# Optimization experiments

Hardware: AMD Instinct MI355X
Metric: run time of the kernel (lower is better)

The kernel has to match this reference:

```python
import jax, jax.numpy as jnp
import numpy as np

N, A, R = 131072, 16, 64


def setup_inputs() -> dict:
    key = jax.random.key(0)
    k1, k2, k3 = jax.random.split(key, 3)
    x = jax.random.normal(k1, (N, A), dtype=jnp.float32)
    mu = jax.random.uniform(k2, (R, A), dtype=jnp.float32)      # torch.rand(R, A)
    sigma = jnp.ones((R, A), dtype=jnp.float32) * 0.2           # torch.ones(R, A) * 0.2
    rho = jax.random.normal(k3, (R, A + 1), dtype=jnp.float32) * 0.1
    return {"x": x, "mu": mu, "sigma": sigma, "rho": rho}


def reference(x, mu, sigma, rho):
    # Rule consequents: z[k, r] = x[k] . rho[r, :A] + rho[r, A]   -> [N, R]
    z = jnp.einsum("na,ra->nr", x, rho[:, :-1]) + rho[:, -1]
    # Gaussian membership firing strengths (prod of exps == exp of sum):
    # w[k, r] = prod_a exp(-(x[k,a]-mu[r,a])^2 / (2 sigma[r,a]^2))
    d = x[:, None, :] - mu[None, :, :]                           # [N, R, A]
    logw = -jnp.sum(d * d / (2.0 * sigma[None] ** 2), axis=-1)   # [N, R]
    w = jnp.exp(logw)
    # diag(z @ w.T)[k] = sum_r z[k,r] * w[k,r]; normalized by rule-sum.
    num = jnp.sum(z * w, axis=1)
    den = jnp.sum(w, axis=1) + 1e-13
    return num / den
```

## Files before the change

### kernel.cpp

```cpp
#include <hip/hip_runtime.h>
#include <math.h>

#define NFEAT 16
#define NRULE 64
#define NCHUNK 19
#define FLAG_DW (NCHUNK * 64 * 4)

typedef _Float16 half8 __attribute__((ext_vector_type(8)));
typedef float    f4    __attribute__((ext_vector_type(4)));
union F4H8 { float4 f; half8 h; };
union F4A  { float4 v; float f[4]; };

__global__ void fuzzy_prep(const float* __restrict__ mu,
                           const float* __restrict__ sigma,
                           const float* __restrict__ rho,
                           float* __restrict__ tab) {
    const float L2E = 1.4426950408889634f;
    __shared__ int u_sh[256];
    int t = threadIdx.x;
    int L = t & 63, T = t >> 6;
    int n = L & 15, quad = L >> 4;
    int rule = T * 16 + n;
    int fb = (quad & 1) * 8;

    F4A M[4], S[4];
    const float4* mup = (const float4*)(mu + rule * NFEAT);
    const float4* sgp = (const float4*)(sigma + rule * NFEAT);
#pragma unroll
    for (int i = 0; i < 4; ++i) { M[i].v = mup[i]; S[i].v = sgp[i]; }

    F4H8 b1, b2, r1, r2;
#pragma unroll
    for (int j = 0; j < 8; ++j) {
        int f = fb + j;
        float m = M[f >> 2].f[f & 3];
        float s = S[f >> 2].f[f & 3];
        float inv = 1.0f / (2.0f * s * s);
        float Bw = 2.0f * inv * m * L2E;
        _Float16 bh = (_Float16)Bw;
        b1.h[j] = bh;
        b2.h[j] = (_Float16)(Bw - (float)bh);
        float Rw = rho[rule * (NFEAT + 1) + f];
        _Float16 rh = (_Float16)Rw;
        r1.h[j] = rh;
        r2.h[j] = (_Float16)(Rw - (float)rh);
    }
    float4* t4 = (float4*)tab;
    t4[(0  + T) * 64 + L] = b1.f;
    t4[(4  + T) * 64 + L] = b2.f;
    t4[(8  + T) * 64 + L] = r1.f;
    t4[(12 + T) * 64 + L] = r2.f;

    float s0 = S[0].f[0];
    float c0 = 1.0f / (2.0f * s0 * s0);
    float K = 0.0f;
    int u = 1;
#pragma unroll
    for (int a = 0; a < NFEAT; ++a) {
        float m = M[a >> 2].f[a & 3];
        float s = S[a >> 2].f[a & 3];
        float inv = 1.0f / (2.0f * s * s);
        if (inv != c0) u = 0;
        K = fmaf(-inv * m, m, K);
    }
    tab[(16 * 64 + L) * 4 + T] = -c0 * L2E;
    tab[(17 * 64 + L) * 4 + T] = K * L2E;
    tab[(18 * 64 + L) * 4 + T] = rho[rule * (NFEAT + 1) + NFEAT];

    u_sh[t] = u;
    __syncthreads();
    if (t < 64) {
        int uu = u_sh[t] & u_sh[t + 64] & u_sh[t + 128] & u_sh[t + 192];
        unsigned long long b = __ballot(uu != 0);
        if (t == 0) tab[FLAG_DW] = (b == ~0ull) ? 1.0f : 0.0f;
    }
}

__global__ __launch_bounds__(256, 4) void fuzzy_main(const float* __restrict__ x,
                                                     const float* __restrict__ tab,
                                                     const float* __restrict__ mu,
                                                     const float* __restrict__ sigma,
                                                     const float* __restrict__ rho,
                                                     float* __restrict__ out, int n) {
    const int tid  = threadIdx.x;
    const int L    = tid & 63;
    const int quad = L >> 4;
    const int wv   = __builtin_amdgcn_readfirstlane(tid >> 6);
    const int flag = __builtin_amdgcn_readfirstlane((int)tab[FLAG_DW]);
    const int m    = L & 15;
    const int fb   = (quad & 1) * 8;

    if (flag) {
        const float4* t4 = (const float4*)tab;
        F4H8 b1[4], b2[4], r1[4], r2[4];
#pragma unroll
        for (int T = 0; T < 4; ++T) {
            b1[T].f = t4[(0  + T) * 64 + L];
            b2[T].f = t4[(4  + T) * 64 + L];
            r1[T].f = t4[(8  + T) * 64 + L];
            r2[T].f = t4[(12 + T) * 64 + L];
        }
        float4 Pq = t4[16 * 64 + L], Kq = t4[17 * 64 + L], Bq = t4[18 * 64 + L];
        float PvA[4]  = {Pq.x, Pq.y, Pq.z, Pq.w};
        float KLvA[4] = {Kq.x, Kq.y, Kq.z, Kq.w};
        float BvA[4]  = {Bq.x, Bq.y, Bq.z, Bq.w};

#pragma unroll
        for (int it = 0; it < 2; ++it) {
            int gt = (blockIdx.x * 4 + wv) * 2 + it;
            int tb = gt * 16;
            if (tb >= n) break;
            const float4* xp = (const float4*)(x + (size_t)(tb + m) * NFEAT + fb);
            float4 xa = xp[0], xb = xp[1];
            float xv[8] = {xa.x, xa.y, xa.z, xa.w, xb.x, xb.y, xb.z, xb.w};
            F4H8 af;
            float qp = 0.0f;
#pragma unroll
            for (int j = 0; j < 8; ++j) {
                _Float16 h = (_Float16)xv[j];
                af.h[j] = (quad < 2) ? h : (_Float16)(xv[j] - (float)h);
                qp = fmaf(xv[j], xv[j], qp);
            }
            float Qf = qp + __shfl_xor(qp, 16);
            float Qr[4];
#pragma unroll
            for (int p = 0; p < 4; ++p) Qr[p] = __shfl(Qf, quad * 4 + p);

            f4 nsum = {0.f, 0.f, 0.f, 0.f}, dsum = {0.f, 0.f, 0.f, 0.f};
#pragma unroll
            for (int T = 0; T < 4; ++T) {
                f4 z4 = {0.f, 0.f, 0.f, 0.f};
                f4 accL = __builtin_amdgcn_mfma_f32_16x16x32_f16(af.h, b1[T].h, z4, 0, 0, 0);
                accL    = __builtin_amdgcn_mfma_f32_16x16x32_f16(af.h, b2[T].h, accL, 0, 0, 0);
                f4 accZ = __builtin_amdgcn_mfma_f32_16x16x32_f16(af.h, r1[T].h, z4, 0, 0, 0);
                accZ    = __builtin_amdgcn_mfma_f32_16x16x32_f16(af.h, r2[T].h, accZ, 0, 0, 0);
#pragma unroll
                for (int p = 0; p < 4; ++p) {
                    float l = fmaf(PvA[T], Qr[p], accL[p] + KLvA[T]);
                    float w = __builtin_amdgcn_exp2f(l);
                    float zf = accZ[p] + BvA[T];
                    nsum[p] = fmaf(zf, w, nsum[p]);
                    dsum[p] += w;
                }
            }
#pragma unroll
            for (int d = 1; d < 16; d <<= 1) {
#pragma unroll
                for (int p = 0; p < 4; ++p) {
                    nsum[p] += __shfl_xor(nsum[p], d);
                    dsum[p] += __shfl_xor(dsum[p], d);
                }
            }
            if ((L & 15) == 0) {
                float4 o;
                o.x = nsum[0] * __builtin_amdgcn_rcpf(dsum[0] + 1e-13f);
                o.y = nsum[1] * __builtin_amdgcn_rcpf(dsum[1] + 1e-13f);
                o.z = nsum[2] * __builtin_amdgcn_rcpf(dsum[2] + 1e-13f);
                o.w = nsum[3] * __builtin_amdgcn_rcpf(dsum[3] + 1e-13f);
                ((float4*)(out + tb))[quad] = o;
            }
        }
    } else {
        const float L2E = 1.4426950408889634f;
#pragma unroll
        for (int it = 0; it < 2; ++it) {
            int gt = (blockIdx.x * 4 + wv) * 2 + it;
            int tb = gt * 16;
            if (tb >= n) break;
            int s = tb + m;
            const float4* xp = (const float4*)(x + (size_t)s * NFEAT);
            float4 a = xp[0], b = xp[1], c = xp[2], d = xp[3];
            float xs[NFEAT] = {a.x,a.y,a.z,a.w, b.x,b.y,b.z,b.w,
                               c.x,c.y,c.z,c.w, d.x,d.y,d.z,d.w};
            float num = 0.0f, den = 0.0f;
            for (int r = quad * 16; r < quad * 16 + 16; ++r) {
                float z = rho[r * (NFEAT + 1) + NFEAT];
                float l = 0.0f;
                for (int aa = 0; aa < NFEAT; ++aa) {
                    float mm = mu[r * NFEAT + aa];
                    float ss = sigma[r * NFEAT + aa];
                    float inv = 1.0f / (2.0f * ss * ss);
                    float dd = xs[aa] - mm;
                    l = fmaf(-inv * dd, dd, l);
                    z = fmaf(rho[r * (NFEAT + 1) + aa], xs[aa], z);
                }
                float w = __builtin_amdgcn_exp2f(l * L2E);
                num = fmaf(z, w, num);
                den += w;
            }
            num += __shfl_xor(num, 16); den += __shfl_xor(den, 16);
            num += __shfl_xor(num, 32); den += __shfl_xor(den, 32);
            if (L < 16) out[tb + L] = num / (den + 1e-13f);
        }
    }
}

extern "C" void kernel_launch(void* const* d_in, const int* in_sizes, int n_in,
                              void* d_out, int out_size, void* d_ws, size_t ws_size,
                              hipStream_t stream) {
    const float* x     = (const float*)d_in[0];
    const float* mu    = (const float*)d_in[1];
    const float* sigma = (const float*)d_in[2];
    const float* rho   = (const float*)d_in[3];
    float* out = (float*)d_out;
    float* tab = (float*)d_ws;

    int n = in_sizes[0] / NFEAT;

    fuzzy_prep<<<1, 256, 0, stream>>>(mu, sigma, rho, tab);
    int blocks = (n + 127) / 128;
    fuzzy_main<<<blocks, 256, 0, stream>>>(x, tab, mu, sigma, rho, out, n);
}
```

Baseline: 70.51 us.

## Fuse parameter prep into main kernel via shared-memory tables

Removes the separate single-block prep kernel and its global workspace table. Each block now recomputes the split-fp16 coefficient tables and the uniform-sigma flag into shared memory, then runs the MFMA path. Samples per wave go from 2 to 4 tiles, which halves the block count and amortises the per-block prep. This saves one launch and the serialisation between the two kernels, at the cost of redundant prep work in every block and an extra barrier.

Result: slower. 74.21 us (+5.2%).

```diff
diff --git a/kernel.cpp b/kernel.cpp
--- a/kernel.cpp
+++ b/kernel.cpp
@@ -4,110 +4,106 @@
 #define NFEAT 16
 #define NRULE 64
 #define NCHUNK 19
-#define FLAG_DW (NCHUNK * 64 * 4)
+#define IT 4
 
 typedef _Float16 half8 __attribute__((ext_vector_type(8)));
 typedef float    f4    __attribute__((ext_vector_type(4)));
 union F4H8 { float4 f; half8 h; };
 union F4A  { float4 v; float f[4]; };
 
-__global__ void fuzzy_prep(const float* __restrict__ mu,
-                           const float* __restrict__ sigma,
-                           const float* __restrict__ rho,
-                           float* __restrict__ tab) {
+__global__ __launch_bounds__(256, 2) void fuzzy_all(const float* __restrict__ x,
+                                                    const float* __restrict__ mu,
+                                                    const float* __restrict__ sigma,
+                                                    const float* __restrict__ rho,
+                                                    float* __restrict__ out, int n) {
     const float L2E = 1.4426950408889634f;
+    __shared__ float4 sh4[NCHUNK * 64];
     __shared__ int u_sh[256];
-    int t = threadIdx.x;
-    int L = t & 63, T = t >> 6;
-    int n = L & 15, quad = L >> 4;
-    int rule = T * 16 + n;
-    int fb = (quad & 1) * 8;
-
-    F4A M[4], S[4];
-    const float4* mup = (const float4*)(mu + rule * NFEAT);
-    const float4* sgp = (const float4*)(sigma + rule * NFEAT);
-#pragma unroll
-    for (int i = 0; i < 4; ++i) { M[i].v = mup[i]; S[i].v = sgp[i]; }
-
-    F4H8 b1, b2, r1, r2;
-#pragma unroll
-    for (int j = 0; j < 8; ++j) {
-        int f = fb + j;
-        float m = M[f >> 2].f[f & 3];
-        float s = S[f >> 2].f[f & 3];
-        float inv = 1.0f / (2.0f * s * s);
-        float Bw = 2.0f * inv * m * L2E;
-        _Float16 bh = (_Float16)Bw;
-        b1.h[j] = bh;
-        b2.h[j] = (_Float16)(Bw - (float)bh);
-        float Rw = rho[rule * (NFEAT + 1) + f];
-        _Float16 rh = (_Float16)Rw;
-        r1.h[j] = rh;
-        r2.h[j] = (_Float16)(Rw - (float)rh);
+    __shared__ float flag_sh;
+
+    const int t    = threadIdx.x;
+    const int L    = t & 63;
+    const int T    = t >> 6;
+    const int m    = L & 15;
+    const int quad = L >> 4;
+    const int rule = T * 16 + m;
+    const int fb   = (quad & 1) * 8;
+
+    {
+        F4A M[4], S[4];
+        const float4* mup = (const float4*)(mu + rule * NFEAT);
+        const float4* sgp = (const float4*)(sigma + rule * NFEAT);
+#pragma unroll
+        for (int i = 0; i < 4; ++i) { M[i].v = mup[i]; S[i].v = sgp[i]; }
+
+        F4H8 b1, b2, r1, r2;
+#pragma unroll
+        for (int j = 0; j < 8; ++j) {
+            int f = fb + j;
+            float mm = M[f >> 2].f[f & 3];
+            float ss = S[f >> 2].f[f & 3];
+            float inv = 1.0f / (2.0f * ss * ss);
+            float Bw = 2.0f * inv * mm * L2E;
+            _Float16 bh = (_Float16)Bw;
+            b1.h[j] = bh;
+            b2.h[j] = (_Float16)(Bw - (float)bh);
+            float Rw = rho[rule * (NFEAT + 1) + f];
+            _Float16 rh = (_Float16)Rw;
+            r1.h[j] = rh;
+            r2.h[j] = (_Float16)(Rw - (float)rh);
+        }
+        sh4[(0  + T) * 64 + L] = b1.f;
+        sh4[(4  + T) * 64 + L] = b2.f;
+        sh4[(8  + T) * 64 + L] = r1.f;
+        sh4[(12 + T) * 64 + L] = r2.f;
+
+        float s0 = S[0].f[0];
+        float c0 = 1.0f / (2.0f * s0 * s0);
+        float K = 0.0f;
+        int u = 1;
+#pragma unroll
+        for (int a = 0; a < NFEAT; ++a) {
+            float mm = M[a >> 2].f[a & 3];
+            float ss = S[a >> 2].f[a & 3];
+            float inv = 1.0f / (2.0f * ss * ss);
+            if (inv != c0) u = 0;
+            K = fmaf(-inv * mm, mm, K);
+        }
+        float* shf = (float*)sh4;
+        shf[(16 * 64 + L) * 4 + T] = -c0 * L2E;
+        shf[(17 * 64 + L) * 4 + T] = K * L2E;
+        shf[(18 * 64 + L) * 4 + T] = rho[rule * (NFEAT + 1) + NFEAT];
+
+        u_sh[t] = u;
     }
-    float4* t4 = (float4*)tab;
-    t4[(0  + T) * 64 + L] = b1.f;
-    t4[(4  + T) * 64 + L] = b2.f;
-    t4[(8  + T) * 64 + L] = r1.f;
-    t4[(12 + T) * 64 + L] = r2.f;
-
-    float s0 = S[0].f[0];
-    float c0 = 1.0f / (2.0f * s0 * s0);
-    float K = 0.0f;
-    int u = 1;
-#pragma unroll
-    for (int a = 0; a < NFEAT; ++a) {
-        float m = M[a >> 2].f[a & 3];
-        float s = S[a >> 2].f[a & 3];
-        float inv = 1.0f / (2.0f * s * s);
-        if (inv != c0) u = 0;
-        K = fmaf(-inv * m, m, K);
-    }
-    tab[(16 * 64 + L) * 4 + T] = -c0 * L2E;
-    tab[(17 * 64 + L) * 4 + T] = K * L2E;
-    tab[(18 * 64 + L) * 4 + T] = rho[rule * (NFEAT + 1) + NFEAT];
-
-    u_sh[t] = u;
     __syncthreads();
     if (t < 64) {
         int uu = u_sh[t] & u_sh[t + 64] & u_sh[t + 128] & u_sh[t + 192];
         unsigned long long b = __ballot(uu != 0);
-        if (t == 0) tab[FLAG_DW] = (b == ~0ull) ? 1.0f : 0.0f;
+        if (t == 0) flag_sh = (b == ~0ull) ? 1.0f : 0.0f;
     }
-}
-
-__global__ __launch_bounds__(256, 4) void fuzzy_main(const float* __restrict__ x,
-                                                     const float* __restrict__ tab,
-                                                     const float* __restrict__ mu,
-                                                     const float* __restrict__ sigma,
-                                                     const float* __restrict__ rho,
-                                                     float* __restrict__ out, int n) {
-    const int tid  = threadIdx.x;
-    const int L    = tid & 63;
-    const int quad = L >> 4;
-    const int wv   = __builtin_amdgcn_readfirstlane(tid >> 6);
-    const int flag = __builtin_amdgcn_readfirstlane((int)tab[FLAG_DW]);
-    const int m    = L & 15;
-    const int fb   = (quad & 1) * 8;
+    __syncthreads();
+
+    const int wv   = __builtin_amdgcn_readfirstlane(T);
+    const int flag = __builtin_amdgcn_readfirstlane((int)flag_sh);
 
     if (flag) {
-        const float4* t4 = (const float4*)tab;
         F4H8 b1[4], b2[4], r1[4], r2[4];
 #pragma unroll
-        for (int T = 0; T < 4; ++T) {
-            b1[T].f = t4[(0  + T) * 64 + L];
-            b2[T].f = t4[(4  + T) * 64 + L];
-            r1[T].f = t4[(8  + T) * 64 + L];
-            r2[T].f = t4[(12 + T) * 64 + L];
-        }
-        float4 Pq = t4[16 * 64 + L], Kq = t4[17 * 64 + L], Bq = t4[18 * 64 + L];
+        for (int Tt = 0; Tt < 4; ++Tt) {
+            b1[Tt].f = sh4[(0  + Tt) * 64 + L];
+            b2[Tt].f = sh4[(4  + Tt) * 64 + L];
+            r1[Tt].f = sh4[(8  + Tt) * 64 + L];
+            r2[Tt].f = sh4[(12 + Tt) * 64 + L];
+        }
+        float4 Pq = sh4[16 * 64 + L], Kq = sh4[17 * 64 + L], Bq = sh4[18 * 64 + L];
         float PvA[4]  = {Pq.x, Pq.y, Pq.z, Pq.w};
         float KLvA[4] = {Kq.x, Kq.y, Kq.z, Kq.w};
         float BvA[4]  = {Bq.x, Bq.y, Bq.z, Bq.w};
 
 #pragma unroll
-        for (int it = 0; it < 2; ++it) {
-            int gt = (blockIdx.x * 4 + wv) * 2 + it;
+        for (int it = 0; it < IT; ++it) {
+            int gt = (blockIdx.x * 4 + wv) * IT + it;
             int tb = gt * 16;
             if (tb >= n) break;
             const float4* xp = (const float4*)(x + (size_t)(tb + m) * NFEAT + fb);
@@ -128,17 +124,17 @@
 
             f4 nsum = {0.f, 0.f, 0.f, 0.f}, dsum = {0.f, 0.f, 0.f, 0.f};
 #pragma unroll
-            for (int T = 0; T < 4; ++T) {
+            for (int Tt = 0; Tt < 4; ++Tt) {
                 f4 z4 = {0.f, 0.f, 0.f, 0.f};
-                f4 accL = __builtin_amdgcn_mfma_f32_16x16x32_f16(af.h, b1[T].h, z4, 0, 0, 0);
-                accL    = __builtin_amdgcn_mfma_f32_16x16x32_f16(af.h, b2[T].h, accL, 0, 0, 0);
-                f4 accZ = __builtin_amdgcn_mfma_f32_16x16x32_f16(af.h, r1[T].h, z4, 0, 0, 0);
-                accZ    = __builtin_amdgcn_mfma_f32_16x16x32_f16(af.h, r2[T].h, accZ, 0, 0, 0);
+                f4 accL = __builtin_amdgcn_mfma_f32_16x16x32_f16(af.h, b1[Tt].h, z4, 0, 0, 0);
+                accL    = __builtin_amdgcn_mfma_f32_16x16x32_f16(af.h, b2[Tt].h, accL, 0, 0, 0);
+                f4 accZ = __builtin_amdgcn_mfma_f32_16x16x32_f16(af.h, r1[Tt].h, z4, 0, 0, 0);
+                accZ    = __builtin_amdgcn_mfma_f32_16x16x32_f16(af.h, r2[Tt].h, accZ, 0, 0, 0);
 #pragma unroll
                 for (int p = 0; p < 4; ++p) {
-                    float l = fmaf(PvA[T], Qr[p], accL[p] + KLvA[T]);
+                    float l = fmaf(PvA[Tt], Qr[p], accL[p] + KLvA[Tt]);
                     float w = __builtin_amdgcn_exp2f(l);
-                    float zf = accZ[p] + BvA[T];
+                    float zf = accZ[p] + BvA[Tt];
                     nsum[p] = fmaf(zf, w, nsum[p]);
                     dsum[p] += w;
                 }
@@ -161,10 +157,9 @@
             }
         }
     } else {
-        const float L2E = 1.4426950408889634f;
-#pragma unroll
-        for (int it = 0; it < 2; ++it) {
-            int gt = (blockIdx.x * 4 + wv) * 2 + it;
+#pragma unroll
+        for (int it = 0; it < IT; ++it) {
+            int gt = (blockIdx.x * 4 + wv) * IT + it;
             int tb = gt * 16;
             if (tb >= n) break;
             int s = tb + m;
@@ -203,11 +198,10 @@
     const float* sigma = (const float*)d_in[2];
     const float* rho   = (const float*)d_in[3];
     float* out = (float*)d_out;
-    float* tab = (float*)d_ws;
+    (void)d_ws; (void)ws_size;
 
     int n = in_sizes[0] / NFEAT;
-
-    fuzzy_prep<<<1, 256, 0, stream>>>(mu, sigma, rho, tab);
-    int blocks = (n + 127) / 128;
-    fuzzy_main<<<blocks, 256, 0, stream>>>(x, tab, mu, sigma, rho, out, n);
+    int samples_per_block = 4 * IT * 16;
+    int blocks = (n + samples_per_block - 1) / samples_per_block;
+    fuzzy_all<<<blocks, 256, 0, stream>>>(x, mu, sigma, rho, out, n);
 }
```
